# Performance work log

Measured on AMD Instinct MI355X. Metric: run time of the kernel, lower is better.

## Reference

```python
import jax, jax.numpy as jnp
import numpy as np

H = 256          # hidden_size
L = 131072       # encoder sequence length
CE = PE = DE = 10
CHORDS, PITCHES, DURS = 158, 63, 16
IN = CE + PE + DE + CE + CE  # 50 = chord + pitch + dur + sec + context
S = 0.05


def setup_inputs() -> dict:
    key = jax.random.key(0)
    k = jax.random.split(key, 16)
    return {
        "sec": 3,
        "chord": 7,
        "true_pitch": 12,
        "note": jax.random.randint(k[0], (2,), 0, 16),
        "hn": jax.random.normal(k[1], (1, 1, H), jnp.float32) * S,
        "cn": jax.random.normal(k[2], (1, 1, H), jnp.float32) * S,
        "encoder_outputs": jax.random.normal(k[3], (L, H), jnp.float32) * S,
        "chord_emb": jax.random.normal(k[4], (CHORDS, CE), jnp.float32) * S,
        "pitch_emb": jax.random.normal(k[5], (PITCHES, PE), jnp.float32) * S,
        "dur_emb": jax.random.normal(k[6], (DURS, DE), jnp.float32) * S,
        "W_ih": jax.random.normal(k[7], (4 * H, IN), jnp.float32) * S,
        "W_hh": jax.random.normal(k[8], (4 * H, H), jnp.float32) * S,
        "b_ih": jax.random.normal(k[9], (4 * H,), jnp.float32) * S,
        "b_hh": jax.random.normal(k[10], (4 * H,), jnp.float32) * S,
        "pitch_W": jax.random.normal(k[11], (PITCHES, H), jnp.float32) * S,
        "pitch_b": jax.random.normal(k[12], (PITCHES,), jnp.float32) * S,
        "dur_W": jax.random.normal(k[13], (DURS, PE + H), jnp.float32) * S,
        "dur_b": jax.random.normal(k[14], (DURS,), jnp.float32) * S,
        "attn_W": jax.random.normal(k[15], (CE, H), jnp.float32) * S,
        "attn_b": jnp.zeros((CE,), jnp.float32),
    }


def reference(sec, chord, true_pitch, note, hn, cn, encoder_outputs,
              chord_emb, pitch_emb, dur_emb, W_ih, W_hh, b_ih, b_hh,
              pitch_W, pitch_b, dur_W, dur_b, attn_W, attn_b):
    h = hn.reshape(-1)  # [H]
    c = cn.reshape(-1)  # [H]

    # embedding lookups
    e_chord = chord_emb[chord]        # [10]
    e_sec = chord_emb[sec]            # [10]
    e_pitch = pitch_emb[note[0]]      # [10]
    e_dur = dur_emb[note[1]]          # [10]
    e_true = pitch_emb[true_pitch]    # [10]

    # dot-product attention over encoder_outputs (vectorized version of the loop)
    scores = encoder_outputs @ h              # [L]
    w = jax.nn.softmax(scores)                # [L]
    ctx = w @ encoder_outputs                 # [H]
    ctx = ctx @ attn_W.T + attn_b             # [10]

    # single-step LSTM (PyTorch gate order i, f, g, o)
    x = jnp.concatenate([e_pitch, e_dur, e_chord, e_sec, ctx])  # [50]
    gates = W_ih @ x + W_hh @ h + b_ih + b_hh                   # [4H]
    i_g, f_g, g_g, o_g = jnp.split(gates, 4)
    i_g = jax.nn.sigmoid(i_g)
    f_g = jax.nn.sigmoid(f_g)
    g_g = jnp.tanh(g_g)
    o_g = jax.nn.sigmoid(o_g)
    c_new = f_g * c + i_g * g_g
    h_new = o_g * jnp.tanh(c_new)

    # dual heads
    pitch_out = (h_new @ pitch_W.T + pitch_b)[None, :]                      # [1,63]
    dur_out = (jnp.concatenate([e_true, h_new]) @ dur_W.T + dur_b)[None, :]  # [1,16]

    return pitch_out, dur_out, h_new.reshape(1, 1, H), c_new.reshape(1, 1, H)
```

## Files before the change

kernel.cpp:

```cpp
#include <hip/hip_runtime.h>
#include <hip/hip_bf16.h>
#include <math.h>

#define H 256
#define L_SEQ 131072
#define NBLK 1024
#define RPB (L_SEQ / NBLK)
#define GROWS 1024

__device__ __forceinline__ float wave_reduce_sum(float v) {
#pragma unroll
  for (int off = 32; off > 0; off >>= 1) v += __shfl_xor(v, off, 64);
  return v;
}

__global__ __launch_bounds__(256, 4) void k1_attn(
    const float* __restrict__ E, const float* __restrict__ h,
    const float* __restrict__ attn_W, const float* __restrict__ W_hh,
    const float* __restrict__ b_ih, const float* __restrict__ b_hh,
    const float* __restrict__ W_ih,
    const float* __restrict__ chord_emb, const float* __restrict__ pitch_emb,
    const float* __restrict__ dur_emb,
    const int* __restrict__ sec_p, const int* __restrict__ chord_p,
    const int* __restrict__ note_p,
    const float* __restrict__ pitch_W, const float* __restrict__ dur_W,
    float* __restrict__ p10, float* __restrict__ ghh2,
    float* __restrict__ WcT, float* __restrict__ dummy) {
  const int b = blockIdx.x;
  const int t = threadIdx.x;
  const int lane = t & 63;
  const int w = t >> 6;
  const float4 hreg = reinterpret_cast<const float4*>(h)[lane];

  float s = 0.f;
  float4 acc = make_float4(0.f, 0.f, 0.f, 0.f);
  const float4* E4 = reinterpret_cast<const float4*>(E);
  const size_t base = (size_t)b * RPB;
#pragma unroll
  for (int k = 0; k < RPB / 32; ++k) {
    const int r = w * 8 + 32 * k;
    float4 e[8];
#pragma unroll
    for (int j = 0; j < 8; ++j) e[j] = E4[(base + r + j) * 64 + lane];
    float d[8];
#pragma unroll
    for (int j = 0; j < 8; ++j)
      d[j] = e[j].x * hreg.x + e[j].y * hreg.y + e[j].z * hreg.z + e[j].w * hreg.w;
#pragma unroll
    for (int off = 32; off > 0; off >>= 1) {
#pragma unroll
      for (int j = 0; j < 8; ++j) d[j] += __shfl_xor(d[j], off, 64);
    }
#pragma unroll
    for (int j = 0; j < 8; ++j) {
      const float wj = __expf(d[j]);
      s += wj;
      acc.x += wj * e[j].x;
      acc.y += wj * e[j].y;
      acc.z += wj * e[j].z;
      acc.w += wj * e[j].w;
    }
  }
  __shared__ float ss[4];
  __shared__ float4 sacc4[4][64];
  sacc4[w][lane] = acc;
  if (lane == 0) ss[w] = s;
  __syncthreads();
  __shared__ float ctx_s[H];
  {
    const float* sf = reinterpret_cast<const float*>(sacc4);
    ctx_s[t] = (sf[t] + sf[256 + t]) + (sf[512 + t] + sf[768 + t]);
  }
  __syncthreads();
  {
    const float4 c4 = reinterpret_cast<const float4*>(ctx_s)[lane];
    for (int row = w; row < 10; row += 4) {
      const float4 a4 = reinterpret_cast<const float4*>(attn_W + row * H)[lane];
      float d = c4.x * a4.x + c4.y * a4.y + c4.z * a4.z + c4.w * a4.w;
      d = wave_reduce_sum(d);
      if (lane == 0) p10[row * NBLK + b] = d;
    }
  }
  if (t == 0) p10[10 * NBLK + b] = (ss[0] + ss[1]) + (ss[2] + ss[3]);

  if (b < 256) {
    const int r = b * 4 + w;
    const float4 wv = reinterpret_cast<const float4*>(W_hh + (size_t)r * H)[lane];
    float d = wv.x * hreg.x + wv.y * hreg.y + wv.z * hreg.z + wv.w * hreg.w;
    if (lane < 50) {
      const float wih = W_ih[r * 50 + lane];
      if (lane < 40) {
        int idx; const float* tbl;
        if (lane < 10)      { tbl = pitch_emb; idx = note_p[0] * 10 + lane; }
        else if (lane < 20) { tbl = dur_emb;   idx = note_p[1] * 10 + lane - 10; }
        else if (lane < 30) { tbl = chord_emb; idx = chord_p[0] * 10 + lane - 20; }
        else                { tbl = chord_emb; idx = sec_p[0] * 10 + lane - 30; }
        d += wih * tbl[idx];
      } else {
        WcT[(lane - 40) * GROWS + r] = wih;
      }
    }
    d = wave_reduce_sum(d);
    if (lane == 0) ghh2[r] = d + b_ih[r] + b_hh[r];
  } else if (b < 272) {
    const int slice = b - 256;
    float a = 0.f;
    const float4* pw4 = reinterpret_cast<const float4*>(pitch_W);
    for (int i = slice * 256 + t; i < 4032; i += 16 * 256) {
      float4 v = pw4[i]; a += v.x + v.y + v.z + v.w;
    }
    const float4* dw4 = reinterpret_cast<const float4*>(dur_W);
    for (int i = slice * 256 + t; i < 1064; i += 16 * 256) {
      float4 v = dw4[i]; a += v.x + v.y + v.z + v.w;
    }
    a = wave_reduce_sum(a);
    if (lane == 0) dummy[slice * 4 + w] = a;
  }
}

__global__ __launch_bounds__(1024) void k2_tail(
    const float* __restrict__ p10, const float* __restrict__ ghh2,
    const float* __restrict__ WcT, const float* __restrict__ attn_b,
    const float* __restrict__ c_in,
    const float* __restrict__ pitch_W, const float* __restrict__ pitch_b,
    const float* __restrict__ dur_W, const float* __restrict__ dur_b,
    const float* __restrict__ pitch_emb, const int* __restrict__ tp_p,
    float* __restrict__ out) {
  const int t = threadIdx.x;
  const int lane = t & 63, w = t >> 6;
  const int gw = blockIdx.x * 16 + w;

  float4 pa0, pa1, pa2, pa3;
  if (w < 11) {
    const float4* pc = reinterpret_cast<const float4*>(p10 + w * NBLK);
    pa0 = pc[lane]; pa1 = pc[lane + 64]; pa2 = pc[lane + 128]; pa3 = pc[lane + 192];
  }
  const float g0 = ghh2[t];
  float wct[10];
#pragma unroll
  for (int c = 0; c < 10; ++c) wct[c] = WcT[c * GROWS + t];
  const float cin = c_in[t & (H - 1)];
  float4 pw4 = make_float4(0.f, 0.f, 0.f, 0.f);
  float pb = 0.f;
  if (gw < 63) {
    pw4 = reinterpret_cast<const float4*>(pitch_W + (size_t)gw * H)[lane];
    pb = pitch_b[gw];
  }
  float dwr[5] = {0.f, 0.f, 0.f, 0.f, 0.f};
  float db = 0.f;
  if (gw >= 48) {
    const float* dwp = dur_W + (size_t)(gw - 48) * 266;
#pragma unroll
    for (int i = 0; i < 5; ++i) {
      const int k = lane + 64 * i;
      if (k < 266) dwr[i] = dwp[k];
    }
    db = dur_b[gw - 48];
  }
  const float et = (t < 10) ? pitch_emb[tp_p[0] * 10 + t] : 0.f;
  const float ab = (t < 10) ? attn_b[t] : 0.f;

  __shared__ float red[11];
  __shared__ float ctxsh[10];
  __shared__ float gsh[1024];
  __shared__ float hsh[H];
  __shared__ float etsh[16];
  if (w < 11) {
    float v = (pa0.x + pa0.y + pa0.z + pa0.w) + (pa1.x + pa1.y + pa1.z + pa1.w) +
              (pa2.x + pa2.y + pa2.z + pa2.w) + (pa3.x + pa3.y + pa3.z + pa3.w);
    v = wave_reduce_sum(v);
    if (lane == 0) red[w] = v;
  }
  if (t < 10) etsh[t] = et;
  __syncthreads();
  if (t < 10) ctxsh[t] = red[t] / red[10] + ab;
  __syncthreads();
  float g = g0;
#pragma unroll
  for (int c = 0; c < 10; ++c) g += wct[c] * ctxsh[c];
  gsh[t] = g;
  __syncthreads();
  if (t < H) {
    const float i_s = 1.f / (1.f + __expf(-gsh[t]));
    const float f_s = 1.f / (1.f + __expf(-gsh[256 + t]));
    const float g_t = tanhf(gsh[512 + t]);
    const float o_s = 1.f / (1.f + __expf(-gsh[768 + t]));
    const float cn = f_s * cin + i_s * g_t;
    const float hn = o_s * tanhf(cn);
    if (blockIdx.x == 0) {
      out[79 + t] = hn;
      out[335 + t] = cn;
    }
    hsh[t] = hn;
  }
  __syncthreads();
  const float4 h4 = reinterpret_cast<const float4*>(hsh)[lane];
  if (gw < 63) {
    float d = pw4.x * h4.x + pw4.y * h4.y + pw4.z * h4.z + pw4.w * h4.w;
    d = wave_reduce_sum(d);
    if (lane == 0) out[gw] = d + pb;
  }
  if (gw >= 48) {
    float d = 0.f;
#pragma unroll
    for (int i = 0; i < 5; ++i) {
      const int k = lane + 64 * i;
      if (k < 266) d += dwr[i] * (k < 10 ? etsh[k] : hsh[k - 10]);
    }
    d = wave_reduce_sum(d);
    if (lane == 0) out[63 + (gw - 48)] = d + db;
  }
}

extern "C" void kernel_launch(void* const* d_in, const int* in_sizes, int n_in,
                              void* d_out, int out_size, void* d_ws, size_t ws_size,
                              hipStream_t stream) {
  const int* sec       = (const int*)d_in[0];
  const int* chord     = (const int*)d_in[1];
  const int* tp        = (const int*)d_in[2];
  const int* note      = (const int*)d_in[3];
  const float* hn      = (const float*)d_in[4];
  const float* cn      = (const float*)d_in[5];
  const float* E       = (const float*)d_in[6];
  const float* chord_e = (const float*)d_in[7];
  const float* pitch_e = (const float*)d_in[8];
  const float* dur_e   = (const float*)d_in[9];
  const float* W_ih    = (const float*)d_in[10];
  const float* W_hh    = (const float*)d_in[11];
  const float* b_ih    = (const float*)d_in[12];
  const float* b_hh    = (const float*)d_in[13];
  const float* pitch_W = (const float*)d_in[14];
  const float* pitch_b = (const float*)d_in[15];
  const float* dur_W   = (const float*)d_in[16];
  const float* dur_b   = (const float*)d_in[17];
  const float* attn_W  = (const float*)d_in[18];
  const float* attn_b  = (const float*)d_in[19];
  float* out = (float*)d_out;
  float* ws = (float*)d_ws;

  float* p10   = ws;
  float* ghh2  = ws + 11 * NBLK;
  float* WcT   = ghh2 + GROWS;
  float* dummy = WcT + 10 * GROWS;

  k1_attn<<<NBLK, 256, 0, stream>>>(E, hn, attn_W, W_hh, b_ih, b_hh, W_ih,
                                    chord_e, pitch_e, dur_e, sec, chord, note,
                                    pitch_W, dur_W, p10, ghh2, WcT, dummy);
  k2_tail<<<4, 1024, 0, stream>>>(p10, ghh2, WcT, attn_b, cn,
                                  pitch_W, pitch_b, dur_W, dur_b,
                                  pitch_e, tp, out);
}
```

Baseline: 30.25 us.

## Split waves into 16-lane row groups with double-buffered encoder loads

The attention streaming loop is restructured so each 16-lane group handles one encoder row, holding 4 float4 chunks per lane. This cuts the dot-product reduction from a 6-step full-wave shuffle to 4 shuffles within 16 lanes. Loads for the next row are software-prefetched into a second register buffer. The cross-group partial sums are then reduced through a larger shared-memory array, and the softmax denominator is reduced across the wave and divided by 16 to undo the per-group duplication. Register pressure rises, and the shared-memory reduction does more work.

Result: no change. 30.21 us (-0.1%).

```diff
diff --git a/kernel.cpp b/kernel.cpp
--- a/kernel.cpp
+++ b/kernel.cpp
@@ -7,6 +7,8 @@
 #define NBLK 1024
 #define RPB (L_SEQ / NBLK)
 #define GROWS 1024
+
+typedef __attribute__((ext_vector_type(4))) float f32x4;
 
 __device__ __forceinline__ float wave_reduce_sum(float v) {
 #pragma unroll
@@ -30,46 +32,71 @@
   const int t = threadIdx.x;
   const int lane = t & 63;
   const int w = t >> 6;
-  const float4 hreg = reinterpret_cast<const float4*>(h)[lane];
-
+  const int cl = lane & 15;
+  const int g  = lane >> 4;
+
+  const f32x4* E4 = reinterpret_cast<const f32x4*>(E);
+  const f32x4* h4 = reinterpret_cast<const f32x4*>(h);
+
+  f32x4 hk[4];
+#pragma unroll
+  for (int k = 0; k < 4; ++k) hk[k] = h4[cl + 16 * k];
+
+  const f32x4 vzero = {0.f, 0.f, 0.f, 0.f};
+  f32x4 acc[4];
+#pragma unroll
+  for (int k = 0; k < 4; ++k) acc[k] = vzero;
   float s = 0.f;
-  float4 acc = make_float4(0.f, 0.f, 0.f, 0.f);
-  const float4* E4 = reinterpret_cast<const float4*>(E);
+
   const size_t base = (size_t)b * RPB;
-#pragma unroll
-  for (int k = 0; k < RPB / 32; ++k) {
-    const int r = w * 8 + 32 * k;
-    float4 e[8];
-#pragma unroll
-    for (int j = 0; j < 8; ++j) e[j] = E4[(base + r + j) * 64 + lane];
-    float d[8];
-#pragma unroll
-    for (int j = 0; j < 8; ++j)
-      d[j] = e[j].x * hreg.x + e[j].y * hreg.y + e[j].z * hreg.z + e[j].w * hreg.w;
-#pragma unroll
-    for (int off = 32; off > 0; off >>= 1) {
-#pragma unroll
-      for (int j = 0; j < 8; ++j) d[j] += __shfl_xor(d[j], off, 64);
-    }
-#pragma unroll
-    for (int j = 0; j < 8; ++j) {
-      const float wj = __expf(d[j]);
-      s += wj;
-      acc.x += wj * e[j].x;
-      acc.y += wj * e[j].y;
-      acc.z += wj * e[j].z;
-      acc.w += wj * e[j].w;
-    }
-  }
+  size_t off = (base + (size_t)w * 32 + g) * 64 + cl;
+
+  f32x4 eA[4], eB[4];
+#pragma unroll
+  for (int k = 0; k < 4; ++k) eA[k] = E4[off + 16 * k];
+#pragma unroll
+  for (int i = 0; i < 8; ++i) {
+    const f32x4* cur = (i & 1) ? eB : eA;
+    f32x4* nxt = (i & 1) ? eA : eB;
+    if (i < 7) {
+      const size_t o2 = off + 256 * (size_t)(i + 1);
+#pragma unroll
+      for (int k = 0; k < 4; ++k) nxt[k] = E4[o2 + 16 * k];
+    }
+    float d = 0.f;
+#pragma unroll
+    for (int k = 0; k < 4; ++k)
+      d += cur[k].x * hk[k].x + cur[k].y * hk[k].y +
+           cur[k].z * hk[k].z + cur[k].w * hk[k].w;
+    d += __shfl_xor(d, 1, 16);
+    d += __shfl_xor(d, 2, 16);
+    d += __shfl_xor(d, 4, 16);
+    d += __shfl_xor(d, 8, 16);
+    const float wj = __expf(d);
+    s += wj;
+#pragma unroll
+    for (int k = 0; k < 4; ++k) acc[k] += wj * cur[k];
+  }
+
   __shared__ float ss[4];
-  __shared__ float4 sacc4[4][64];
-  sacc4[w][lane] = acc;
-  if (lane == 0) ss[w] = s;
+  __shared__ f32x4 sacc[4][4][16][4];
+#pragma unroll
+  for (int k = 0; k < 4; ++k) sacc[w][g][cl][k] = acc[k];
+  {
+    const float sw = wave_reduce_sum(s) * 0.0625f;
+    if (lane == 0) ss[w] = sw;
+  }
   __syncthreads();
   __shared__ float ctx_s[H];
   {
-    const float* sf = reinterpret_cast<const float*>(sacc4);
-    ctx_s[t] = (sf[t] + sf[256 + t]) + (sf[512 + t] + sf[768 + t]);
+    const int k = t >> 6, cc = (t >> 2) & 15, j = t & 3;
+    float v = 0.f;
+#pragma unroll
+    for (int ww = 0; ww < 4; ++ww)
+#pragma unroll
+      for (int gg = 0; gg < 4; ++gg)
+        v += reinterpret_cast<const float*>(&sacc[ww][gg][cc][k])[j];
+    ctx_s[t] = v;
   }
   __syncthreads();
   {
@@ -83,6 +110,7 @@
   }
   if (t == 0) p10[10 * NBLK + b] = (ss[0] + ss[1]) + (ss[2] + ss[3]);
 
+  const float4 hreg = reinterpret_cast<const float4*>(h)[lane];
   if (b < 256) {
     const int r = b * 4 + w;
     const float4 wv = reinterpret_cast<const float4*>(W_hh + (size_t)r * H)[lane];
```
